# Kernel optimization log

Hardware: AMD Instinct MI355X
Metric: run time of the kernel (lower is better)

Reference implementation:

```python
import jax, jax.numpy as jnp
import numpy as np

F = 128   # flattened observation features
H = 64    # MLP/LSTM hidden size (hardcoded in module)
A = 15    # number of discrete actions
T = 128   # rollout length (timesteps)
B = 2048  # number of parallel envs (batch)


def setup_inputs() -> dict:
    key = jax.random.key(0)
    ks = jax.random.split(key, 12)
    n = lambda k, sh, s=1.0: jax.random.normal(k, sh, jnp.float32) * s
    return {
        "x": n(ks[0], (T * B, F)),
        "done": (jax.random.uniform(ks[1], (T * B,)) < 0.05).astype(jnp.float32),
        "h0": n(ks[2], (1, B, H)),
        "c0": n(ks[3], (1, B, H)),
        # MLP encoder params (Linear stores y = x @ W + b here, W: [in, out])
        "W1": n(ks[4], (F, H), 0.1), "b1": jnp.zeros((H,), jnp.float32),
        "W2": n(ks[5], (H, H), 0.1), "b2": jnp.zeros((H,), jnp.float32),
        # LSTM params, PyTorch layout: weight_ih [4H, H_in], gate order i,f,g,o
        "Wih": n(ks[6], (4 * H, H), 0.1), "bih": jnp.zeros((4 * H,), jnp.float32),
        "Whh": n(ks[7], (4 * H, H), 0.1), "bhh": jnp.zeros((4 * H,), jnp.float32),
        # actor / critic heads
        "Wa": n(ks[8], (H, A), 0.01), "ba": jnp.zeros((A,), jnp.float32),
        "Wc": n(ks[9], (H, 1), 1.0), "bc": jnp.zeros((1,), jnp.float32),
    }


def reference(x, done, h0, c0, W1, b1, W2, b2, Wih, bih, Whh, bhh, Wa, ba, Wc, bc):
    Bsz, Hh = h0.shape[1], h0.shape[2]
    # MLP encoder: Linear -> Tanh -> Linear -> Tanh
    y = jnp.tanh(x @ W1 + b1)
    y = jnp.tanh(y @ W2 + b2)                 # [T*B, H]
    y = y.reshape(-1, Bsz, Hh)                # [T, B, H]
    d = done.reshape(-1, Bsz)                 # [T, B]

    def step(carry, td):
        h, c = carry
        yt, dt = td
        m = (1.0 - dt)[:, None]               # done-mask hidden reset
        h = h * m
        c = c * m
        g = yt @ Wih.T + bih + h @ Whh.T + bhh  # [B, 4H]
        i, f, gg, o = jnp.split(g, 4, axis=-1)
        c = jax.nn.sigmoid(f) * c + jax.nn.sigmoid(i) * jnp.tanh(gg)
        h = jax.nn.sigmoid(o) * jnp.tanh(c)
        return (h, c), h

    (hT, cT), outs = jax.lax.scan(step, (h0[0], c0[0]), (y, d))
    z = outs.reshape(-1, Hh)                  # [T*B, H]
    logits = z @ Wa + ba                      # Categorical logits
    vf = z @ Wc + bc
    return logits, vf, hT[None], cT[None]
```

## Files before the change

kernel.cpp:

```cpp
#include <hip/hip_runtime.h>
#include <hip/hip_bf16.h>
#include <stdint.h>

typedef __bf16  bf16x8 __attribute__((ext_vector_type(8)));
typedef short   s16x8  __attribute__((ext_vector_type(8)));
typedef short   s16x4  __attribute__((ext_vector_type(4)));
typedef int     i32x4  __attribute__((ext_vector_type(4)));
typedef float   f32x4  __attribute__((ext_vector_type(4)));

union Frag { s16x8 s; bf16x8 b; i32x4 i; };

static __device__ __forceinline__ short f2bf(float f) {
    union { float f; unsigned u; } v; v.f = f;
    unsigned r = (v.u + 0x7FFFu + ((v.u >> 16) & 1u)) >> 16;
    return (short)r;
}
static __device__ __forceinline__ float bf2f(short s) {
    union { unsigned u; float f; } v; v.u = ((unsigned)(unsigned short)s) << 16;
    return v.f;
}
static __device__ __forceinline__ float fast_rcp(float x) { return __builtin_amdgcn_rcpf(x); }
static __device__ __forceinline__ float sigm(float x) { return fast_rcp(1.0f + __expf(-x)); }
static __device__ __forceinline__ float tanh_fast(float x) {
    float e = __expf(-2.0f * x);
    return (1.0f - e) * fast_rcp(1.0f + e);
}
static __device__ __forceinline__ f32x4 mfma16(bf16x8 a, bf16x8 b, f32x4 c) {
    return __builtin_amdgcn_mfma_f32_16x16x32_bf16(a, b, c, 0, 0, 0);
}

#define GLDS(gp, lp) __builtin_amdgcn_global_load_lds( \
    (const __attribute__((address_space(1))) void*)(gp), \
    (__attribute__((address_space(3))) void*)(lp), 16, 0, 0)

#define BAR_LGKM() asm volatile("s_waitcnt lgkmcnt(0)\n\ts_barrier" ::: "memory")
#define BAR_ALL()  asm volatile("s_waitcnt vmcnt(0) lgkmcnt(0)\n\ts_barrier" ::: "memory")

#define TT 128
#define BB 2048
#define HH 64
#define FF 128
#define AA 15
#define YR 32
#define LOGITS_OFF 0
#define VF_OFF   3932160
#define HT_OFF   4194304
#define CT_OFF   4325376


__global__ __launch_bounds__(256) void enc_kernel(
    const float* __restrict__ x, const float* __restrict__ W1, const float* __restrict__ b1,
    const float* __restrict__ W2, const float* __restrict__ b2, short* __restrict__ y_sw)
{
    __shared__ short w1t[64][136];
    __shared__ short w2t[64][72];
    __shared__ short c1buf[4][16][72];
    __shared__ short ybuf[4][16][72];

    const int tid  = threadIdx.x;
    const int lane = tid & 63;
    const int w    = tid >> 6;
    const int c    = lane & 15;
    const int q    = lane >> 4;

    for (int i = tid; i < 128*64; i += 256) { int k = i >> 6, n = i & 63; w1t[n][k] = f2bf(W1[i]); }
    for (int i = tid; i < 64*64;  i += 256) { int k = i >> 6, n = i & 63; w2t[n][k] = f2bf(W2[i]); }

    float b1v[4], b2v[4];
#pragma unroll
    for (int ct = 0; ct < 4; ++ct) { b1v[ct] = b1[16*ct + c]; b2v[ct] = b2[16*ct + c]; }
    __syncthreads();

    for (int it = 0; it < 4; ++it) {
        const int wt = it*4096 + blockIdx.x*4 + w;
        const int r0 = wt * 16;
        Frag af[4];
#pragma unroll
        for (int kf = 0; kf < 4; ++kf) {
            const float* xp = x + (size_t)(r0 + c)*FF + 32*kf + 8*q;
            f32x4 x0 = *(const f32x4*)xp;
            f32x4 x1 = *(const f32x4*)(xp + 4);
#pragma unroll
            for (int jj = 0; jj < 4; ++jj) { af[kf].s[jj] = f2bf(x0[jj]); af[kf].s[4+jj] = f2bf(x1[jj]); }
        }
        f32x4 acc[4];
#pragma unroll
        for (int ct = 0; ct < 4; ++ct) acc[ct] = (f32x4){b1v[ct], b1v[ct], b1v[ct], b1v[ct]};
#pragma unroll
        for (int kf = 0; kf < 4; ++kf)
#pragma unroll
            for (int ct = 0; ct < 4; ++ct) {
                Frag bf; bf.s = *(const s16x8*)&w1t[16*ct + c][32*kf + 8*q];
                acc[ct] = mfma16(af[kf].b, bf.b, acc[ct]);
            }
#pragma unroll
        for (int ct = 0; ct < 4; ++ct)
#pragma unroll
            for (int i = 0; i < 4; ++i)
                c1buf[w][4*q + i][16*ct + c] = f2bf(tanh_fast(acc[ct][i]));
        Frag a2[2];
#pragma unroll
        for (int kf = 0; kf < 2; ++kf) a2[kf].s = *(const s16x8*)&c1buf[w][c][32*kf + 8*q];
        f32x4 acc2[4];
#pragma unroll
        for (int ct = 0; ct < 4; ++ct) acc2[ct] = (f32x4){b2v[ct], b2v[ct], b2v[ct], b2v[ct]};
#pragma unroll
        for (int kf = 0; kf < 2; ++kf)
#pragma unroll
            for (int ct = 0; ct < 4; ++ct) {
                Frag bf; bf.s = *(const s16x8*)&w2t[16*ct + c][32*kf + 8*q];
                acc2[ct] = mfma16(a2[kf].b, bf.b, acc2[ct]);
            }
#pragma unroll
        for (int ct = 0; ct < 4; ++ct)
#pragma unroll
            for (int i = 0; i < 4; ++i)
                ybuf[w][4*q + i][16*ct + c] = f2bf(tanh_fast(acc2[ct][i]));
#pragma unroll
        for (int kf = 0; kf < 2; ++kf) {
            s16x8 yv = *(const s16x8*)&ybuf[w][c][32*kf + 8*q];
            *(s16x8*)(y_sw + (size_t)wt*1024 + kf*512 + lane*8) = yv;
        }
    }
}

__global__ __launch_bounds__(256, 1) void scan_kernel(
    const short* __restrict__ y_sw, const float* __restrict__ done,
    const float* __restrict__ h0, const float* __restrict__ c0,
    const float* __restrict__ Wih, const float* __restrict__ bih,
    const float* __restrict__ Whh, const float* __restrict__ bhh,
    const float* __restrict__ Wa, const float* __restrict__ ba,
    const float* __restrict__ Wc, const float* __restrict__ bc,
    float* __restrict__ out_logits, float* __restrict__ out_vf,
    float* __restrict__ hT_out, float* __restrict__ cT_out)
{
    __shared__ short ybig[YR][1024];
    __shared__ short zbuf[2][16][72];
    __shared__ float dbuf[TT][16];
    __shared__ float obuf[2][8][16][16];

    const int tid  = threadIdx.x;
    const int lane = tid & 63;
    const int w    = tid >> 6;
    const int c    = lane & 15;
    const int q    = lane >> 4;
    const int blk  = blockIdx.x;
    const int b0   = blk * 16;

    Frag  wfr[4][4];
    f32x4 biasv[4];
#pragma unroll
    for (int a = 0; a < 4; ++a) {
        const int gc = 64*a + 16*w + c;
#pragma unroll
        for (int kf = 0; kf < 4; ++kf) {
            const float* wp = (kf < 2) ? (Wih + (size_t)gc*HH + 32*kf + 8*q)
                                       : (Whh + (size_t)gc*HH + 32*(kf-2) + 8*q);
            f32x4 w0 = *(const f32x4*)wp;
            f32x4 w1 = *(const f32x4*)(wp + 4);
#pragma unroll
            for (int jj = 0; jj < 4; ++jj) { wfr[a][kf].s[jj] = f2bf(w0[jj]); wfr[a][kf].s[4+jj] = f2bf(w1[jj]); }
        }
        const int bcol = 64*a + 16*w + 4*q;
        biasv[a] = *(const f32x4*)(bih + bcol);
        f32x4 b2 = *(const f32x4*)(bhh + bcol);
#pragma unroll
        for (int jj = 0; jj < 4; ++jj) biasv[a][jj] += b2[jj];
    }
    Frag hwf[2];
#pragma unroll
    for (int kf = 0; kf < 2; ++kf)
#pragma unroll
        for (int jj = 0; jj < 8; ++jj) {
            int k = 32*kf + 8*q + jj;
            hwf[kf].s[jj] = f2bf((c < 15) ? Wa[k*AA + c] : Wc[k]);
        }
    const float hbv = (c < 15) ? ba[c] : bc[0];

    f32x4 cst = *(const f32x4*)(c0 + (size_t)(b0 + c)*HH + 16*w + 4*q);

    {
        int r = tid & 15, c4 = (tid >> 4) * 4;
        f32x4 hv = *(const f32x4*)(h0 + (size_t)(b0 + r)*HH + c4);
        s16x4 hp;
#pragma unroll
        for (int ii = 0; ii < 4; ++ii) hp[ii] = f2bf(hv[ii]);
        *(s16x4*)&zbuf[1][r][c4] = hp;
    }
#pragma unroll
    for (int i = 0; i < 2; ++i) {
        int j = w*2 + i;
        const float* gp = done + (size_t)(16*j + (lane >> 2))*BB + b0 + 4*(lane & 3);
        GLDS(gp, &dbuf[16*j][0]);
    }
    for (int s = w; s < 31; s += 4)
#pragma unroll
        for (int half = 0; half < 2; ++half) {
            const short* gp = y_sw + ((size_t)s*128 + blk)*1024 + half*512 + lane*8;
            GLDS(gp, &ybig[s][half*512]);
        }
    BAR_ALL();

    f32x4 hv;

    for (int t = 0; t < TT; ++t) {
        const int rb = (t + 1) & 1, wb = t & 1, slot = t & (YR-1);
        Frag z0, z1, y0, y1;
        z0.s = *(const s16x8*)&zbuf[rb][c][8*q];
        z1.s = *(const s16x8*)&zbuf[rb][c][32 + 8*q];
        y0.s = *(const s16x8*)&ybig[slot][lane*8];
        y1.s = *(const s16x8*)&ybig[slot][512 + lane*8];
        const float dme = dbuf[t][c];
        if (w == (t & 3) && t <= TT-32) {
            const int ds = (t + 31) & (YR-1);
#pragma unroll
            for (int half = 0; half < 2; ++half) {
                const short* gp = y_sw + ((size_t)(t+31)*128 + blk)*1024 + half*512 + lane*8;
                GLDS(gp, &ybig[ds][half*512]);
            }
        }
        if (t > 0 && w == (t & 3)) {
            f32x4 ha = (f32x4){hbv, hbv, hbv, hbv};
            ha = mfma16(z0.b, hwf[0].b, ha);
            ha = mfma16(z1.b, hwf[1].b, ha);
            const int tp = t - 1;
#pragma unroll
            for (int i = 0; i < 4; ++i)
                obuf[(tp >> 3) & 1][tp & 7][4*q + i][c] = ha[i];
        }
        const int msk = (dme != 0.0f) ? 0 : -1;
        Frag zm0, zm1;
#pragma unroll
        for (int k = 0; k < 4; ++k) { zm0.i[k] = z0.i[k] & msk; zm1.i[k] = z1.i[k] & msk; }
        f32x4 acc[4];
#pragma unroll
        for (int a = 0; a < 4; ++a) {
            acc[a] = biasv[a];
            acc[a] = mfma16(wfr[a][0].b, y0.b,  acc[a]);
            acc[a] = mfma16(wfr[a][1].b, y1.b,  acc[a]);
            acc[a] = mfma16(wfr[a][2].b, zm0.b, acc[a]);
            acc[a] = mfma16(wfr[a][3].b, zm1.b, acc[a]);
        }
#pragma unroll
        for (int i = 0; i < 4; ++i) {
            float cm = (dme != 0.0f) ? 0.0f : cst[i];
            float cn = sigm(acc[1][i])*cm + sigm(acc[0][i])*tanh_fast(acc[2][i]);
            cst[i] = cn;
            hv[i]  = sigm(acc[3][i])*tanh_fast(cn);
        }
        {
            s16x4 hp;
#pragma unroll
            for (int ii = 0; ii < 4; ++ii) hp[ii] = f2bf(hv[ii]);
            *(s16x4*)&zbuf[wb][c][16*w + 4*q] = hp;
        }
        if ((t & 7) == 1 && t > 8 && lane < 32) {
            const int cc = (t >> 3) - 1;
            const int idx = w*32 + lane;
            const int s = idx >> 4, r = idx & 15;
            const float* ob = &obuf[cc & 1][s][r][0];
            f32x4 o0 = *(const f32x4*)ob,     o1 = *(const f32x4*)(ob+4);
            f32x4 o2 = *(const f32x4*)(ob+8), o3 = *(const f32x4*)(ob+12);
            const size_t row = (size_t)(8*cc + s)*BB + b0 + r;
            float* lp = out_logits + row*AA;
            lp[0]=o0[0]; lp[1]=o0[1]; lp[2]=o0[2]; lp[3]=o0[3];
            lp[4]=o1[0]; lp[5]=o1[1]; lp[6]=o1[2]; lp[7]=o1[3];
            lp[8]=o2[0]; lp[9]=o2[1]; lp[10]=o2[2]; lp[11]=o2[3];
            lp[12]=o3[0]; lp[13]=o3[1]; lp[14]=o3[2];
            out_vf[row] = o3[3];
        }
        BAR_LGKM();
    }

    if (w == 3) {
        Frag z0, z1;
        z0.s = *(const s16x8*)&zbuf[1][c][8*q];
        z1.s = *(const s16x8*)&zbuf[1][c][32 + 8*q];
        f32x4 ha = (f32x4){hbv, hbv, hbv, hbv};
        ha = mfma16(z0.b, hwf[0].b, ha);
        ha = mfma16(z1.b, hwf[1].b, ha);
#pragma unroll
        for (int i = 0; i < 4; ++i) obuf[1][7][4*q + i][c] = ha[i];
    }
    BAR_LGKM();
    if (lane < 32) {
        const int idx = w*32 + lane;
        const int s = idx >> 4, r = idx & 15;
        const float* ob = &obuf[1][s][r][0];
        f32x4 o0 = *(const f32x4*)ob,     o1 = *(const f32x4*)(ob+4);
        f32x4 o2 = *(const f32x4*)(ob+8), o3 = *(const f32x4*)(ob+12);
        const size_t row = (size_t)(120 + s)*BB + b0 + r;
        float* lp = out_logits + row*AA;
        lp[0]=o0[0]; lp[1]=o0[1]; lp[2]=o0[2]; lp[3]=o0[3];
        lp[4]=o1[0]; lp[5]=o1[1]; lp[6]=o1[2]; lp[7]=o1[3];
        lp[8]=o2[0]; lp[9]=o2[1]; lp[10]=o2[2]; lp[11]=o2[3];
        lp[12]=o3[0]; lp[13]=o3[1]; lp[14]=o3[2];
        out_vf[row] = o3[3];
    }
    *(f32x4*)(hT_out + (size_t)(b0 + c)*HH + 16*w + 4*q) = hv;
    *(f32x4*)(cT_out + (size_t)(b0 + c)*HH + 16*w + 4*q) = cst;
}

extern "C" void kernel_launch(void* const* d_in, const int* in_sizes, int n_in,
                              void* d_out, int out_size, void* d_ws, size_t ws_size,
                              hipStream_t stream) {
    const float* x    = (const float*)d_in[0];
    const float* done = (const float*)d_in[1];
    const float* h0   = (const float*)d_in[2];
    const float* c0   = (const float*)d_in[3];
    const float* W1   = (const float*)d_in[4];
    const float* b1   = (const float*)d_in[5];
    const float* W2   = (const float*)d_in[6];
    const float* b2   = (const float*)d_in[7];
    const float* Wih  = (const float*)d_in[8];
    const float* bih  = (const float*)d_in[9];
    const float* Whh  = (const float*)d_in[10];
    const float* bhh  = (const float*)d_in[11];
    const float* Wa   = (const float*)d_in[12];
    const float* ba   = (const float*)d_in[13];
    const float* Wc   = (const float*)d_in[14];
    const float* bc   = (const float*)d_in[15];
    float* out = (float*)d_out;

    short* y_sw = (short*)d_ws;

    enc_kernel<<<1024, 256, 0, stream>>>(x, W1, b1, W2, b2, y_sw);
    scan_kernel<<<128, 256, 0, stream>>>(y_sw, done, h0, c0, Wih, bih, Whh, bhh,
                                         Wa, ba, Wc, bc,
                                         out + LOGITS_OFF, out + VF_OFF,
                                         out + HT_OFF, out + CT_OFF);
}
```

Baseline: 326.7 us.

## Move heads out of LSTM scan and precompute input projection off critical path

The actor/critic head matmuls leave the serial scan loop. The scan now writes bf16 hidden states to workspace, and a separate heads_kernel computes logits and value in parallel afterwards. Inside the scan, the input-projection MFMAs for step t+1 are issued after the current h update, so only the recurrent half stays on the dependency chain. The encoder is also relaunched with 4x more blocks and no inner loop. The cost is an extra workspace round trip for z, one more kernel launch, and output stores from the heads kernel that are less coalesced.

```diff
diff --git a/kernel.cpp b/kernel.cpp
--- a/kernel.cpp
+++ b/kernel.cpp
@@ -14,10 +14,6 @@
     union { float f; unsigned u; } v; v.f = f;
     unsigned r = (v.u + 0x7FFFu + ((v.u >> 16) & 1u)) >> 16;
     return (short)r;
-}
-static __device__ __forceinline__ float bf2f(short s) {
-    union { unsigned u; float f; } v; v.u = ((unsigned)(unsigned short)s) << 16;
-    return v.f;
 }
 static __device__ __forceinline__ float fast_rcp(float x) { return __builtin_amdgcn_rcpf(x); }
 static __device__ __forceinline__ float sigm(float x) { return fast_rcp(1.0f + __expf(-x)); }
@@ -71,56 +67,54 @@
     for (int ct = 0; ct < 4; ++ct) { b1v[ct] = b1[16*ct + c]; b2v[ct] = b2[16*ct + c]; }
     __syncthreads();
 
-    for (int it = 0; it < 4; ++it) {
-        const int wt = it*4096 + blockIdx.x*4 + w;
-        const int r0 = wt * 16;
-        Frag af[4];
-#pragma unroll
-        for (int kf = 0; kf < 4; ++kf) {
-            const float* xp = x + (size_t)(r0 + c)*FF + 32*kf + 8*q;
-            f32x4 x0 = *(const f32x4*)xp;
-            f32x4 x1 = *(const f32x4*)(xp + 4);
-#pragma unroll
-            for (int jj = 0; jj < 4; ++jj) { af[kf].s[jj] = f2bf(x0[jj]); af[kf].s[4+jj] = f2bf(x1[jj]); }
-        }
-        f32x4 acc[4];
-#pragma unroll
-        for (int ct = 0; ct < 4; ++ct) acc[ct] = (f32x4){b1v[ct], b1v[ct], b1v[ct], b1v[ct]};
-#pragma unroll
-        for (int kf = 0; kf < 4; ++kf)
-#pragma unroll
-            for (int ct = 0; ct < 4; ++ct) {
-                Frag bf; bf.s = *(const s16x8*)&w1t[16*ct + c][32*kf + 8*q];
-                acc[ct] = mfma16(af[kf].b, bf.b, acc[ct]);
-            }
-#pragma unroll
-        for (int ct = 0; ct < 4; ++ct)
-#pragma unroll
-            for (int i = 0; i < 4; ++i)
-                c1buf[w][4*q + i][16*ct + c] = f2bf(tanh_fast(acc[ct][i]));
-        Frag a2[2];
-#pragma unroll
-        for (int kf = 0; kf < 2; ++kf) a2[kf].s = *(const s16x8*)&c1buf[w][c][32*kf + 8*q];
-        f32x4 acc2[4];
-#pragma unroll
-        for (int ct = 0; ct < 4; ++ct) acc2[ct] = (f32x4){b2v[ct], b2v[ct], b2v[ct], b2v[ct]};
-#pragma unroll
-        for (int kf = 0; kf < 2; ++kf)
-#pragma unroll
-            for (int ct = 0; ct < 4; ++ct) {
-                Frag bf; bf.s = *(const s16x8*)&w2t[16*ct + c][32*kf + 8*q];
-                acc2[ct] = mfma16(a2[kf].b, bf.b, acc2[ct]);
-            }
-#pragma unroll
-        for (int ct = 0; ct < 4; ++ct)
-#pragma unroll
-            for (int i = 0; i < 4; ++i)
-                ybuf[w][4*q + i][16*ct + c] = f2bf(tanh_fast(acc2[ct][i]));
-#pragma unroll
-        for (int kf = 0; kf < 2; ++kf) {
-            s16x8 yv = *(const s16x8*)&ybuf[w][c][32*kf + 8*q];
-            *(s16x8*)(y_sw + (size_t)wt*1024 + kf*512 + lane*8) = yv;
-        }
+    const int wt = blockIdx.x*4 + w;
+    const int r0 = wt * 16;
+    Frag af[4];
+#pragma unroll
+    for (int kf = 0; kf < 4; ++kf) {
+        const float* xp = x + (size_t)(r0 + c)*FF + 32*kf + 8*q;
+        f32x4 x0 = *(const f32x4*)xp;
+        f32x4 x1 = *(const f32x4*)(xp + 4);
+#pragma unroll
+        for (int jj = 0; jj < 4; ++jj) { af[kf].s[jj] = f2bf(x0[jj]); af[kf].s[4+jj] = f2bf(x1[jj]); }
+    }
+    f32x4 acc[4];
+#pragma unroll
+    for (int ct = 0; ct < 4; ++ct) acc[ct] = (f32x4){b1v[ct], b1v[ct], b1v[ct], b1v[ct]};
+#pragma unroll
+    for (int kf = 0; kf < 4; ++kf)
+#pragma unroll
+        for (int ct = 0; ct < 4; ++ct) {
+            Frag bf; bf.s = *(const s16x8*)&w1t[16*ct + c][32*kf + 8*q];
+            acc[ct] = mfma16(af[kf].b, bf.b, acc[ct]);
+        }
+#pragma unroll
+    for (int ct = 0; ct < 4; ++ct)
+#pragma unroll
+        for (int i = 0; i < 4; ++i)
+            c1buf[w][4*q + i][16*ct + c] = f2bf(tanh_fast(acc[ct][i]));
+    Frag a2[2];
+#pragma unroll
+    for (int kf = 0; kf < 2; ++kf) a2[kf].s = *(const s16x8*)&c1buf[w][c][32*kf + 8*q];
+    f32x4 acc2[4];
+#pragma unroll
+    for (int ct = 0; ct < 4; ++ct) acc2[ct] = (f32x4){b2v[ct], b2v[ct], b2v[ct], b2v[ct]};
+#pragma unroll
+    for (int kf = 0; kf < 2; ++kf)
+#pragma unroll
+        for (int ct = 0; ct < 4; ++ct) {
+            Frag bf; bf.s = *(const s16x8*)&w2t[16*ct + c][32*kf + 8*q];
+            acc2[ct] = mfma16(a2[kf].b, bf.b, acc2[ct]);
+        }
+#pragma unroll
+    for (int ct = 0; ct < 4; ++ct)
+#pragma unroll
+        for (int i = 0; i < 4; ++i)
+            ybuf[w][4*q + i][16*ct + c] = f2bf(tanh_fast(acc2[ct][i]));
+#pragma unroll
+    for (int kf = 0; kf < 2; ++kf) {
+        s16x8 yv = *(const s16x8*)&ybuf[w][c][32*kf + 8*q];
+        *(s16x8*)(y_sw + (size_t)wt*1024 + kf*512 + lane*8) = yv;
     }
 }
 
@@ -129,15 +123,11 @@
     const float* __restrict__ h0, const float* __restrict__ c0,
     const float* __restrict__ Wih, const float* __restrict__ bih,
     const float* __restrict__ Whh, const float* __restrict__ bhh,
-    const float* __restrict__ Wa, const float* __restrict__ ba,
-    const float* __restrict__ Wc, const float* __restrict__ bc,
-    float* __restrict__ out_logits, float* __restrict__ out_vf,
-    float* __restrict__ hT_out, float* __restrict__ cT_out)
+    short* __restrict__ z_g, float* __restrict__ hT_out, float* __restrict__ cT_out)
 {
     __shared__ short ybig[YR][1024];
-    __shared__ short zbuf[2][16][72];
+    __shared__ short hbuf[2][16][72];
     __shared__ float dbuf[TT][16];
-    __shared__ float obuf[2][8][16][16];
 
     const int tid  = threadIdx.x;
     const int lane = tid & 63;
@@ -163,29 +153,18 @@
         }
         const int bcol = 64*a + 16*w + 4*q;
         biasv[a] = *(const f32x4*)(bih + bcol);
-        f32x4 b2 = *(const f32x4*)(bhh + bcol);
-#pragma unroll
-        for (int jj = 0; jj < 4; ++jj) biasv[a][jj] += b2[jj];
-    }
-    Frag hwf[2];
-#pragma unroll
-    for (int kf = 0; kf < 2; ++kf)
-#pragma unroll
-        for (int jj = 0; jj < 8; ++jj) {
-            int k = 32*kf + 8*q + jj;
-            hwf[kf].s[jj] = f2bf((c < 15) ? Wa[k*AA + c] : Wc[k]);
-        }
-    const float hbv = (c < 15) ? ba[c] : bc[0];
-
+        f32x4 bx = *(const f32x4*)(bhh + bcol);
+#pragma unroll
+        for (int jj = 0; jj < 4; ++jj) biasv[a][jj] += bx[jj];
+    }
     f32x4 cst = *(const f32x4*)(c0 + (size_t)(b0 + c)*HH + 16*w + 4*q);
-
     {
         int r = tid & 15, c4 = (tid >> 4) * 4;
-        f32x4 hv = *(const f32x4*)(h0 + (size_t)(b0 + r)*HH + c4);
+        f32x4 hvv = *(const f32x4*)(h0 + (size_t)(b0 + r)*HH + c4);
         s16x4 hp;
 #pragma unroll
-        for (int ii = 0; ii < 4; ++ii) hp[ii] = f2bf(hv[ii]);
-        *(s16x4*)&zbuf[1][r][c4] = hp;
+        for (int ii = 0; ii < 4; ++ii) hp[ii] = f2bf(hvv[ii]);
+        *(s16x4*)&hbuf[1][r][c4] = hp;
     }
 #pragma unroll
     for (int i = 0; i < 2; ++i) {
@@ -201,44 +180,33 @@
         }
     BAR_ALL();
 
+    float dme = dbuf[0][c];
+    f32x4 g2[4];
+    {
+        Frag y0, y1;
+        y0.s = *(const s16x8*)&ybig[0][lane*8];
+        y1.s = *(const s16x8*)&ybig[0][512 + lane*8];
+#pragma unroll
+        for (int a = 0; a < 4; ++a) {
+            g2[a] = mfma16(wfr[a][0].b, y0.b, biasv[a]);
+            g2[a] = mfma16(wfr[a][1].b, y1.b, g2[a]);
+        }
+    }
     f32x4 hv;
 
     for (int t = 0; t < TT; ++t) {
-        const int rb = (t + 1) & 1, wb = t & 1, slot = t & (YR-1);
-        Frag z0, z1, y0, y1;
-        z0.s = *(const s16x8*)&zbuf[rb][c][8*q];
-        z1.s = *(const s16x8*)&zbuf[rb][c][32 + 8*q];
-        y0.s = *(const s16x8*)&ybig[slot][lane*8];
-        y1.s = *(const s16x8*)&ybig[slot][512 + lane*8];
-        const float dme = dbuf[t][c];
-        if (w == (t & 3) && t <= TT-32) {
-            const int ds = (t + 31) & (YR-1);
-#pragma unroll
-            for (int half = 0; half < 2; ++half) {
-                const short* gp = y_sw + ((size_t)(t+31)*128 + blk)*1024 + half*512 + lane*8;
-                GLDS(gp, &ybig[ds][half*512]);
-            }
-        }
-        if (t > 0 && w == (t & 3)) {
-            f32x4 ha = (f32x4){hbv, hbv, hbv, hbv};
-            ha = mfma16(z0.b, hwf[0].b, ha);
-            ha = mfma16(z1.b, hwf[1].b, ha);
-            const int tp = t - 1;
-#pragma unroll
-            for (int i = 0; i < 4; ++i)
-                obuf[(tp >> 3) & 1][tp & 7][4*q + i][c] = ha[i];
-        }
+        const int rb = (t + 1) & 1, wb = t & 1;
+        Frag hf0, hf1;
+        hf0.s = *(const s16x8*)&hbuf[rb][c][8*q];
+        hf1.s = *(const s16x8*)&hbuf[rb][c][32 + 8*q];
         const int msk = (dme != 0.0f) ? 0 : -1;
         Frag zm0, zm1;
 #pragma unroll
-        for (int k = 0; k < 4; ++k) { zm0.i[k] = z0.i[k] & msk; zm1.i[k] = z1.i[k] & msk; }
+        for (int k = 0; k < 4; ++k) { zm0.i[k] = hf0.i[k] & msk; zm1.i[k] = hf1.i[k] & msk; }
         f32x4 acc[4];
 #pragma unroll
         for (int a = 0; a < 4; ++a) {
-            acc[a] = biasv[a];
-            acc[a] = mfma16(wfr[a][0].b, y0.b,  acc[a]);
-            acc[a] = mfma16(wfr[a][1].b, y1.b,  acc[a]);
-            acc[a] = mfma16(wfr[a][2].b, zm0.b, acc[a]);
+            acc[a] = mfma16(wfr[a][2].b, zm0.b, g2[a]);
             acc[a] = mfma16(wfr[a][3].b, zm1.b, acc[a]);
         }
 #pragma unroll
@@ -248,57 +216,75 @@
             cst[i] = cn;
             hv[i]  = sigm(acc[3][i])*tanh_fast(cn);
         }
-        {
-            s16x4 hp;
-#pragma unroll
-            for (int ii = 0; ii < 4; ++ii) hp[ii] = f2bf(hv[ii]);
-            *(s16x4*)&zbuf[wb][c][16*w + 4*q] = hp;
-        }
-        if ((t & 7) == 1 && t > 8 && lane < 32) {
-            const int cc = (t >> 3) - 1;
-            const int idx = w*32 + lane;
-            const int s = idx >> 4, r = idx & 15;
-            const float* ob = &obuf[cc & 1][s][r][0];
-            f32x4 o0 = *(const f32x4*)ob,     o1 = *(const f32x4*)(ob+4);
-            f32x4 o2 = *(const f32x4*)(ob+8), o3 = *(const f32x4*)(ob+12);
-            const size_t row = (size_t)(8*cc + s)*BB + b0 + r;
-            float* lp = out_logits + row*AA;
-            lp[0]=o0[0]; lp[1]=o0[1]; lp[2]=o0[2]; lp[3]=o0[3];
-            lp[4]=o1[0]; lp[5]=o1[1]; lp[6]=o1[2]; lp[7]=o1[3];
-            lp[8]=o2[0]; lp[9]=o2[1]; lp[10]=o2[2]; lp[11]=o2[3];
-            lp[12]=o3[0]; lp[13]=o3[1]; lp[14]=o3[2];
-            out_vf[row] = o3[3];
+        s16x4 hp;
+#pragma unroll
+        for (int ii = 0; ii < 4; ++ii) hp[ii] = f2bf(hv[ii]);
+        *(s16x4*)&hbuf[wb][c][16*w + 4*q] = hp;
+        *(s16x4*)(z_g + ((size_t)t*128 + blk)*1024 + c*64 + 16*w + 4*q) = hp;
+        if (t < TT-1) {
+            Frag yn0, yn1;
+            yn0.s = *(const s16x8*)&ybig[(t+1) & (YR-1)][lane*8];
+            yn1.s = *(const s16x8*)&ybig[(t+1) & (YR-1)][512 + lane*8];
+            dme = dbuf[t+1][c];
+#pragma unroll
+            for (int a = 0; a < 4; ++a) {
+                g2[a] = mfma16(wfr[a][0].b, yn0.b, biasv[a]);
+                g2[a] = mfma16(wfr[a][1].b, yn1.b, g2[a]);
+            }
+        }
+        if (w == (t & 3) && t <= TT-32) {
+            const int ds = (t + 31) & (YR-1);
+#pragma unroll
+            for (int half = 0; half < 2; ++half) {
+                const short* gp = y_sw + ((size_t)(t+31)*128 + blk)*1024 + half*512 + lane*8;
+                GLDS(gp, &ybig[ds][half*512]);
+            }
         }
         BAR_LGKM();
-    }
-
-    if (w == 3) {
-        Frag z0, z1;
-        z0.s = *(const s16x8*)&zbuf[1][c][8*q];
-        z1.s = *(const s16x8*)&zbuf[1][c][32 + 8*q];
-        f32x4 ha = (f32x4){hbv, hbv, hbv, hbv};
-        ha = mfma16(z0.b, hwf[0].b, ha);
-        ha = mfma16(z1.b, hwf[1].b, ha);
-#pragma unroll
-        for (int i = 0; i < 4; ++i) obuf[1][7][4*q + i][c] = ha[i];
-    }
-    BAR_LGKM();
-    if (lane < 32) {
-        const int idx = w*32 + lane;
-        const int s = idx >> 4, r = idx & 15;
-        const float* ob = &obuf[1][s][r][0];
-        f32x4 o0 = *(const f32x4*)ob,     o1 = *(const f32x4*)(ob+4);
-        f32x4 o2 = *(const f32x4*)(ob+8), o3 = *(const f32x4*)(ob+12);
-        const size_t row = (size_t)(120 + s)*BB + b0 + r;
-        float* lp = out_logits + row*AA;
-        lp[0]=o0[0]; lp[1]=o0[1]; lp[2]=o0[2]; lp[3]=o0[3];
-        lp[4]=o1[0]; lp[5]=o1[1]; lp[6]=o1[2]; lp[7]=o1[3];
-        lp[8]=o2[0]; lp[9]=o2[1]; lp[10]=o2[2]; lp[11]=o2[3];
-        lp[12]=o3[0]; lp[13]=o3[1]; lp[14]=o3[2];
-        out_vf[row] = o3[3];
     }
     *(f32x4*)(hT_out + (size_t)(b0 + c)*HH + 16*w + 4*q) = hv;
     *(f32x4*)(cT_out + (size_t)(b0 + c)*HH + 16*w + 4*q) = cst;
+}
+
+__global__ __launch_bounds__(256) void heads_kernel(
+    const short* __restrict__ z_g, const float* __restrict__ Wa, const float* __restrict__ ba,
+    const float* __restrict__ Wc, const float* __restrict__ bc,
+    float* __restrict__ out_logits, float* __restrict__ out_vf)
+{
+    const int tid  = threadIdx.x;
+    const int lane = tid & 63;
+    const int w    = tid >> 6;
+    const int c    = lane & 15;
+    const int q    = lane >> 4;
+
+    Frag hwf[2];
+#pragma unroll
+    for (int kf = 0; kf < 2; ++kf)
+#pragma unroll
+        for (int jj = 0; jj < 8; ++jj) {
+            int k = 32*kf + 8*q + jj;
+            hwf[kf].s[jj] = f2bf((c < 15) ? Wa[k*AA + c] : Wc[k]);
+        }
+    const float bv = (c < 15) ? ba[c] : bc[0];
+
+    for (int s = 0; s < 4; ++s) {
+        const int wt = s*4096 + blockIdx.x*4 + w;
+        const short* zt = z_g + (size_t)wt*1024;
+        Frag b0, b1;
+        b0.s = *(const s16x8*)(zt + c*64 + 8*q);
+        b1.s = *(const s16x8*)(zt + c*64 + 32 + 8*q);
+        f32x4 acc = (f32x4){bv, bv, bv, bv};
+        acc = mfma16(hwf[0].b, b0.b, acc);
+        acc = mfma16(hwf[1].b, b1.b, acc);
+        const size_t row = (size_t)wt*16 + c;
+        float* lp = out_logits + row*AA + 4*q;
+        if (q < 3) {
+            lp[0]=acc[0]; lp[1]=acc[1]; lp[2]=acc[2]; lp[3]=acc[3];
+        } else {
+            lp[0]=acc[0]; lp[1]=acc[1]; lp[2]=acc[2];
+            out_vf[row] = acc[3];
+        }
+    }
 }
 
 extern "C" void kernel_launch(void* const* d_in, const int* in_sizes, int n_in,
@@ -323,10 +309,11 @@
     float* out = (float*)d_out;
 
     short* y_sw = (short*)d_ws;
-
-    enc_kernel<<<1024, 256, 0, stream>>>(x, W1, b1, W2, b2, y_sw);
+    short* z_g  = y_sw + 16777216;
+
+    enc_kernel<<<4096, 256, 0, stream>>>(x, W1, b1, W2, b2, y_sw);
     scan_kernel<<<128, 256, 0, stream>>>(y_sw, done, h0, c0, Wih, bih, Whh, bhh,
-                                         Wa, ba, Wc, bc,
-                                         out + LOGITS_OFF, out + VF_OFF,
-                                         out + HT_OFF, out + CT_OFF);
-}
+                                         z_g, out + HT_OFF, out + CT_OFF);
+    heads_kernel<<<1024, 256, 0, stream>>>(z_g, Wa, ba, Wc, bc,
+                                           out + LOGITS_OFF, out + VF_OFF);
+}
```

Measured after the change: 335.1 us. 1.03x slower.
